# Kernel optimization log

Measured on AMD Instinct MI355X. Metric: run time of the kernel, lower is better.

## Reference

```python
import jax, jax.numpy as jnp
import numpy as np
from jax import lax

N, C_IN, C_OUT, H, W = 8, 64, 64, 128, 128
K, KS, STRIDE, PAD, GROUPS = 4, 3, 1, 1, 1


def setup_inputs() -> dict:
    key = jax.random.key(0)
    ks = jax.random.split(key, 10)
    s = 0.05
    return {
        "x": jax.random.normal(ks[0], (N, C_IN, H, W), jnp.float32),
        "weight": jax.random.normal(ks[1], (K, C_OUT, C_IN // GROUPS, KS, KS), jnp.float32) * s,
        "conv_w": jax.random.normal(ks[2], (C_OUT, C_IN, KS, KS), jnp.float32) * s,
        "conv_b": jax.random.normal(ks[3], (C_OUT,), jnp.float32) * s,
        "net0_w": jax.random.normal(ks[4], (K, 1, 1, 1, 1), jnp.float32) * s,
        "net0_b": jax.random.normal(ks[5], (K,), jnp.float32) * s,
        "net1_w": jax.random.normal(ks[6], (K, 1, 3, 3, 3), jnp.float32) * s,
        "net1_b": jax.random.normal(ks[7], (K,), jnp.float32) * s,
        "net2_w": jax.random.normal(ks[8], (K, 1, 5, 3, 3), jnp.float32) * s,
        "net2_b": jax.random.normal(ks[9], (K,), jnp.float32) * s,
    }


def _conv3d_mean(x5, w, b, pad):
    # x5: (N,1,C,H,W); w: (K,1,kd,kh,kw); 'same'-style padding per kernel.
    y = lax.conv_general_dilated(x5, w, (1, 1, 1), [(p, p) for p in pad],
                                 dimension_numbers=('NCDHW', 'OIDHW', 'NCDHW'))
    # global avg pool over (C,H,W); bias is constant so add after the mean.
    return jnp.mean(y, axis=(2, 3, 4)) + b[None, :]


def reference(x, weight, conv_w, conv_b, net0_w, net0_b, net1_w, net1_b, net2_w, net2_b):
    dn2 = ('NCHW', 'OIHW', 'NCHW')
    # static residual conv branch
    r = lax.conv_general_dilated(x, conv_w, (STRIDE, STRIDE), [(PAD, PAD)] * 2,
                                 dimension_numbers=dn2) + conv_b[None, :, None, None]
    # attention over 3D convs of x.unsqueeze(1)
    x5 = x[:, None]  # (N,1,C,H,W)
    logits = (_conv3d_mean(x5, net0_w, net0_b, (0, 0, 0))
              + _conv3d_mean(x5, net1_w, net1_b, (1, 1, 1))
              + _conv3d_mean(x5, net2_w, net2_b, (2, 1, 1)))  # (N,K)
    att = jax.nn.softmax(logits, axis=-1)
    # per-sample dynamic kernel mixing: (N,K) @ (K,out,in/g,kh,kw)
    agg_w = jnp.einsum('nk,koihw->noihw', att, weight)
    # grouped conv with groups = GROUPS*N == per-sample conv (vmapped)
    def per_sample(xi, wi):
        return lax.conv_general_dilated(xi[None], wi, (STRIDE, STRIDE), [(PAD, PAD)] * 2,
                                        dimension_numbers=dn2,
                                        feature_group_count=GROUPS)[0]
    out = jax.vmap(per_sample)(x, agg_w)  # (N,out,H,W)
    return out + r
```

## Files before the change

### kernel.cpp

```cpp
#include <hip/hip_runtime.h>


typedef unsigned short ushort_t;
typedef __attribute__((ext_vector_type(8))) short bf16x8;
typedef __attribute__((ext_vector_type(4))) float f32x4;

__device__ __forceinline__ ushort_t f2bf(float f) {
    unsigned u = __float_as_uint(f);
    unsigned r = (u + 0x7fffu + ((u >> 16) & 1u)) >> 16;
    return (ushort_t)r;
}

__global__ __launch_bounds__(256) void kTR(const float* __restrict__ x,
                                           ushort_t* __restrict__ xt,
                                           float* __restrict__ part) {
    int row = blockIdx.x;
    int h = row & 127, n = row >> 7;
    int tid = threadIdx.x;
    int wg = tid & 31;
    int ci8 = tid >> 5;

    __shared__ float catloc[15];
    if (tid < 15) catloc[tid] = 0.f;
    __syncthreads();

    const float* xp = x + (size_t)(n * 64 + ci8 * 8) * 16384 + h * 128 + wg;
    float v[8][4];
#pragma unroll
    for (int j = 0; j < 8; ++j)
#pragma unroll
        for (int c = 0; c < 4; ++c)
            v[j][c] = xp[j * 16384 + c * 32];

    ushort_t* op = xt + ((size_t)(row * 8 + ci8)) * 128 * 8;
#pragma unroll
    for (int c = 0; c < 4; ++c) {
        ushort_t u[8];
#pragma unroll
        for (int j = 0; j < 8; ++j) u[j] = f2bf(v[j][c]);
        uint4 pk;
        pk.x = (unsigned)u[0] | ((unsigned)u[1] << 16);
        pk.y = (unsigned)u[2] | ((unsigned)u[3] << 16);
        pk.z = (unsigned)u[4] | ((unsigned)u[5] << 16);
        pk.w = (unsigned)u[6] | ((unsigned)u[7] << 16);
        *(uint4*)(op + (size_t)(wg + c * 32) * 8) = pk;
    }

#pragma unroll
    for (int j = 0; j < 8; ++j) {
        float rs = v[j][0] + v[j][1] + v[j][2] + v[j][3];
#pragma unroll
        for (int m = 1; m <= 16; m <<= 1) rs += __shfl_xor(rs, m);
        int ci = ci8 * 8 + j;
        int cd = (ci == 0) ? 0 : (ci == 1) ? 1 : (ci == 62) ? 3 : (ci == 63) ? 4 : 2;
        if (wg == 0) {
            atomicAdd(&catloc[cd * 3 + 0], rs);
            atomicAdd(&catloc[cd * 3 + 1], v[j][0]);
        }
        if (wg == 31) atomicAdd(&catloc[cd * 3 + 2], v[j][3]);
    }
    __syncthreads();
    if (tid < 15) part[row * 16 + tid] = catloc[tid];
}

__global__ __launch_bounds__(256) void kW(const float* __restrict__ part,
                                          const float* __restrict__ nw0, const float* __restrict__ nb0,
                                          const float* __restrict__ nw1, const float* __restrict__ nb1,
                                          const float* __restrict__ nw2, const float* __restrict__ nb2,
                                          const float* __restrict__ weight,
                                          const float* __restrict__ convw,
                                          ushort_t* __restrict__ weff) {
    int bid = blockIdx.x;
    int s = bid % 9;
    int n = bid / 9;
    int tid = threadIdx.x;

    __shared__ float cat_s[45];
    __shared__ float box_s[45];
    __shared__ float tot_s;
    __shared__ float att_s[4];

    if (tid < 45) cat_s[tid] = 0.f;
    __syncthreads();
    if (tid < 128) {
        int h = tid;
        int ch = (h == 0) ? 0 : (h == 127) ? 2 : 1;
        const float* pp = part + (size_t)(n * 128 + h) * 16;
#pragma unroll
        for (int q = 0; q < 15; ++q) {
            int cd = q / 3, st = q % 3;
            atomicAdd(&cat_s[(cd * 3 + ch) * 3 + st], pp[q]);
        }
    }
    __syncthreads();

    if (tid < 46) {
        float c[5][3][3];
#pragma unroll
        for (int i = 0; i < 5; ++i)
#pragma unroll
            for (int j = 0; j < 3; ++j)
#pragma unroll
                for (int t = 0; t < 3; ++t)
                    c[i][j][t] = cat_s[(i * 3 + j) * 3 + t];

        if (tid < 45) {
            int dz = tid / 9 - 2;
            int dy = (tid / 3) % 3 - 1;
            int dx = tid % 3 - 1;
            float acc = 0.f;
#pragma unroll
            for (int cd = 0; cd < 5; ++cd) {
                int dv = (cd == 0) ? 0 : (cd == 1) ? 1 : (cd == 3) ? 62 : (cd == 4) ? 63 : -1;
                bool incd = (dv < 0) || (dv >= dz && dv < 64 + dz);
#pragma unroll
                for (int ch = 0; ch < 3; ++ch) {
                    int hv = (ch == 0) ? 0 : (ch == 2) ? 127 : -1;
                    bool inch = (hv < 0) || (hv >= dy && hv < 128 + dy);
                    if (incd && inch) {
                        float v = c[cd][ch][0];
                        if (dx == -1) v -= c[cd][ch][2];
                        else if (dx == 1) v -= c[cd][ch][1];
                        acc += v;
                    }
                }
            }
            box_s[tid] = acc;
        } else {
            float tot = 0.f;
#pragma unroll
            for (int i = 0; i < 5; ++i)
#pragma unroll
                for (int j = 0; j < 3; ++j) tot += c[i][j][0];
            tot_s = tot;
        }
    }
    __syncthreads();

    if (tid < 4) {
        int k = tid;
        const float invV = 1.0f / (64.f * 128.f * 128.f);
        float lg = nb0[k] + nb1[k] + nb2[k] + nw0[k] * tot_s * invV;
#pragma unroll
        for (int dz = 0; dz < 3; ++dz)
#pragma unroll
            for (int dy = 0; dy < 3; ++dy)
#pragma unroll
                for (int dx = 0; dx < 3; ++dx)
                    lg += nw1[k * 27 + dz * 9 + dy * 3 + dx] *
                          box_s[(dz + 1) * 9 + dy * 3 + dx] * invV;
#pragma unroll
        for (int b = 0; b < 45; ++b)
            lg += nw2[k * 45 + b] * box_s[b] * invV;

        float m = fmaxf(lg, __shfl_xor(lg, 1));
        m = fmaxf(m, __shfl_xor(m, 2));
        float e = __expf(lg - m);
        float ssum = e + __shfl_xor(e, 1);
        ssum += __shfl_xor(ssum, 2);
        att_s[k] = e / ssum;
    }
    __syncthreads();

    float a0 = att_s[0], a1 = att_s[1], a2 = att_s[2], a3 = att_s[3];
    int ci = tid & 63;
    int cog = tid >> 6;
    ushort_t* wp = weff + ((size_t)(n * 9 + s) * 64) * 64;
#pragma unroll
    for (int p = 0; p < 16; ++p) {
        int co = cog * 16 + p;
        size_t base = (size_t)(co * 64 + ci) * 9 + s;
        float v = convw[base]
                + a0 * weight[base]
                + a1 * weight[base +     64 * 64 * 9]
                + a2 * weight[base + 2 * 64 * 64 * 9]
                + a3 * weight[base + 3 * 64 * 64 * 9];
        wp[(size_t)co * 64 + ci] = f2bf(v);
    }
}

__global__ __launch_bounds__(256, 2) void kC(const ushort_t* __restrict__ xt,
                                             const ushort_t* __restrict__ weff,
                                             const float* __restrict__ convb,
                                             float* __restrict__ out) {
    int bid = blockIdx.x;
    int wt = bid & 1;
    int hq = (bid >> 1) & 31;
    int n = bid >> 6;
    int h0 = hq * 4;
    int w0 = wt * 64;

    __shared__ __align__(16) ushort_t lds[6 * 8 * 66 * 8];

    int tid = threadIdx.x;
    int lane = tid & 63;
    int wave = tid >> 6;
    int kq = lane >> 4;
    int l15 = lane & 15;

    for (int idx = tid; idx < 3168; idx += 256) {
        int c = idx % 66;
        int rc8 = idx / 66;
        int r = rc8 >> 3, ci8 = rc8 & 7;
        int hg = h0 + r - 1;
        int wg = w0 + c - 1;
        uint4 vv = make_uint4(0u, 0u, 0u, 0u);
        if (hg >= 0 && hg < 128 && wg >= 0 && wg < 128)
            vv = *(const uint4*)(xt + ((size_t)((n * 128 + hg) * 8 + ci8) * 128 + wg) * 8);
        *(uint4*)&lds[(size_t)idx * 8] = vv;
    }

    int co_a = wave * 16 + l15;
    bf16x8 afrag[9][2];
#pragma unroll
    for (int s = 0; s < 9; ++s)
#pragma unroll
        for (int kc = 0; kc < 2; ++kc)
            afrag[s][kc] = *(const bf16x8*)(weff +
                ((size_t)((n * 9 + s) * 64 + co_a)) * 64 + kc * 32 + kq * 8);

    f32x4 acc[16];
#pragma unroll
    for (int t = 0; t < 16; ++t) acc[t] = (f32x4){0.f, 0.f, 0.f, 0.f};

    __syncthreads();

#pragma unroll
    for (int kx = 0; kx < 3; ++kx) {
#pragma unroll
        for (int kc = 0; kc < 2; ++kc) {
#pragma unroll
            for (int col = 0; col < 4; ++col) {
                bf16x8 brow[6];
#pragma unroll
                for (int p = 0; p < 6; ++p)
                    brow[p] = *(const bf16x8*)
                        &lds[(((p * 8 + kc * 4 + kq) * 66) + col * 16 + l15 + kx) * 8];
#pragma unroll
                for (int ky = 0; ky < 3; ++ky)
#pragma unroll
                    for (int r = 0; r < 4; ++r)
                        acc[r * 4 + col] = __builtin_amdgcn_mfma_f32_16x16x32_bf16(
                            afrag[ky * 3 + kx][kc], brow[r + ky], acc[r * 4 + col], 0, 0, 0);
            }
        }
    }

#pragma unroll
    for (int r = 0; r < 4; ++r) {
        int h = h0 + r;
#pragma unroll
        for (int col = 0; col < 4; ++col) {
            int w = w0 + col * 16 + l15;
#pragma unroll
            for (int reg = 0; reg < 4; ++reg) {
                int co = wave * 16 + kq * 4 + reg;
                float v = acc[r * 4 + col][reg] + convb[co];
                out[(((size_t)n * 64 + co) * 128 + h) * 128 + w] = v;
            }
        }
    }
}

extern "C" void kernel_launch(void* const* d_in, const int* in_sizes, int n_in,
                              void* d_out, int out_size, void* d_ws, size_t ws_size,
                              hipStream_t stream) {
    const float* x      = (const float*)d_in[0];
    const float* weight = (const float*)d_in[1];
    const float* conv_w = (const float*)d_in[2];
    const float* conv_b = (const float*)d_in[3];
    const float* n0w    = (const float*)d_in[4];
    const float* n0b    = (const float*)d_in[5];
    const float* n1w    = (const float*)d_in[6];
    const float* n1b    = (const float*)d_in[7];
    const float* n2w    = (const float*)d_in[8];
    const float* n2b    = (const float*)d_in[9];
    float* out = (float*)d_out;

    char* ws = (char*)d_ws;
    ushort_t* xt   = (ushort_t*)(ws);
    ushort_t* weff = (ushort_t*)(ws + 16777216);
    float*    part = (float*)(ws + 16777216 + 589824);

    kTR<<<1024, 256, 0, stream>>>(x, xt, part);
    kW<<<72, 256, 0, stream>>>(part, n0w, n0b, n1w, n1b, n2w, n2b,
                               weight, conv_w, weff);
    kC<<<512, 256, 0, stream>>>(xt, weff, conv_b, out);
}
```

Measured before the change: 130.4 us.

## Pre-pad transposed input and use direct global-to-LDS loads in conv kernel

The transposed bf16 input is now stored with a zero border of width one in H and W (130x130), written by the transpose kernel. The conv kernel can then drop its bounds checks and stage its tile with global_load_lds buffer-to-LDS transfers that skip registers, with a short register-path tail. The weight-mixing kernel is split across four times as many blocks (each handles a quarter of the output channels), and conv blocks are reordered so batch varies fastest. The trade-offs are extra border writes, a larger workspace, and kW blocks that each redo the attention reduction.

```diff
diff --git a/kernel.cpp b/kernel.cpp
--- a/kernel.cpp
+++ b/kernel.cpp
@@ -9,6 +9,12 @@
     unsigned u = __float_as_uint(f);
     unsigned r = (u + 0x7fffu + ((u >> 16) & 1u)) >> 16;
     return (ushort_t)r;
+}
+
+__device__ __forceinline__ void gl_lds16(const ushort_t* g, ushort_t* l) {
+    __builtin_amdgcn_global_load_lds(
+        (const __attribute__((address_space(1))) unsigned*)g,
+        (__attribute__((address_space(3))) unsigned*)l, 16, 0, 0);
 }
 
 __global__ __launch_bounds__(256) void kTR(const float* __restrict__ x,
@@ -32,7 +38,7 @@
         for (int c = 0; c < 4; ++c)
             v[j][c] = xp[j * 16384 + c * 32];
 
-    ushort_t* op = xt + ((size_t)(row * 8 + ci8)) * 128 * 8;
+    ushort_t* op = xt + (((size_t)(n * 130 + h + 1) * 8 + ci8) * 130 + 1) * 8;
 #pragma unroll
     for (int c = 0; c < 4; ++c) {
         ushort_t u[8];
@@ -44,6 +50,18 @@
         pk.z = (unsigned)u[4] | ((unsigned)u[5] << 16);
         pk.w = (unsigned)u[6] | ((unsigned)u[7] << 16);
         *(uint4*)(op + (size_t)(wg + c * 32) * 8) = pk;
+    }
+
+    if (tid < 16) {
+        int cib = tid & 7, side = tid >> 3;
+        *(uint4*)(xt + (((size_t)(n * 130 + h + 1) * 8 + cib) * 130 + side * 129) * 8)
+            = make_uint4(0u, 0u, 0u, 0u);
+    }
+    if (h == 0 || h == 127) {
+        int hp = (h == 0) ? 0 : 129;
+        size_t base = (size_t)(n * 130 + hp) * 8 * 130;
+        for (int ii = tid; ii < 1040; ii += 256)
+            *(uint4*)(xt + (base + ii) * 8) = make_uint4(0u, 0u, 0u, 0u);
     }
 
 #pragma unroll
@@ -71,8 +89,10 @@
                                           const float* __restrict__ convw,
                                           ushort_t* __restrict__ weff) {
     int bid = blockIdx.x;
-    int s = bid % 9;
-    int n = bid / 9;
+    int q = bid & 3;
+    int ns = bid >> 2;
+    int s = ns % 9;
+    int n = ns / 9;
     int tid = threadIdx.x;
 
     __shared__ float cat_s[45];
@@ -87,9 +107,9 @@
         int ch = (h == 0) ? 0 : (h == 127) ? 2 : 1;
         const float* pp = part + (size_t)(n * 128 + h) * 16;
 #pragma unroll
-        for (int q = 0; q < 15; ++q) {
-            int cd = q / 3, st = q % 3;
-            atomicAdd(&cat_s[(cd * 3 + ch) * 3 + st], pp[q]);
+        for (int p = 0; p < 15; ++p) {
+            int cd = p / 3, st = p % 3;
+            atomicAdd(&cat_s[(cd * 3 + ch) * 3 + st], pp[p]);
         }
     }
     __syncthreads();
@@ -118,10 +138,10 @@
                     int hv = (ch == 0) ? 0 : (ch == 2) ? 127 : -1;
                     bool inch = (hv < 0) || (hv >= dy && hv < 128 + dy);
                     if (incd && inch) {
-                        float v = c[cd][ch][0];
-                        if (dx == -1) v -= c[cd][ch][2];
-                        else if (dx == 1) v -= c[cd][ch][1];
-                        acc += v;
+                        float vv = c[cd][ch][0];
+                        if (dx == -1) vv -= c[cd][ch][2];
+                        else if (dx == 1) vv -= c[cd][ch][1];
+                        acc += vv;
                     }
                 }
             }
@@ -167,8 +187,8 @@
     int cog = tid >> 6;
     ushort_t* wp = weff + ((size_t)(n * 9 + s) * 64) * 64;
 #pragma unroll
-    for (int p = 0; p < 16; ++p) {
-        int co = cog * 16 + p;
+    for (int p = 0; p < 4; ++p) {
+        int co = cog * 16 + q * 4 + p;
         size_t base = (size_t)(co * 64 + ci) * 9 + s;
         float v = convw[base]
                 + a0 * weight[base]
@@ -183,10 +203,11 @@
                                              const ushort_t* __restrict__ weff,
                                              const float* __restrict__ convb,
                                              float* __restrict__ out) {
-    int bid = blockIdx.x;
-    int wt = bid & 1;
-    int hq = (bid >> 1) & 31;
-    int n = bid >> 6;
+    int b = blockIdx.x;
+    int n = b & 7;
+    int r2 = b >> 3;
+    int wt = r2 & 1;
+    int hq = r2 >> 1;
     int h0 = hq * 4;
     int w0 = wt * 64;
 
@@ -198,16 +219,22 @@
     int kq = lane >> 4;
     int l15 = lane & 15;
 
-    for (int idx = tid; idx < 3168; idx += 256) {
-        int c = idx % 66;
-        int rc8 = idx / 66;
-        int r = rc8 >> 3, ci8 = rc8 & 7;
-        int hg = h0 + r - 1;
-        int wg = w0 + c - 1;
-        uint4 vv = make_uint4(0u, 0u, 0u, 0u);
-        if (hg >= 0 && hg < 128 && wg >= 0 && wg < 128)
-            vv = *(const uint4*)(xt + ((size_t)((n * 128 + hg) * 8 + ci8) * 128 + wg) * 8);
-        *(uint4*)&lds[(size_t)idx * 8] = vv;
+    size_t sbase = ((size_t)(n * 130 + h0) * 8) * 130 + w0;
+#pragma unroll
+    for (int m = 0; m < 12; ++m) {
+        int chunk = m * 256 + tid;
+        int c = chunk % 66;
+        int rc8 = chunk / 66;
+        size_t so = sbase + (size_t)(rc8 >> 3) * 1040 + (size_t)(rc8 & 7) * 130 + c;
+        gl_lds16(xt + so * 8, &lds[(size_t)chunk * 8]);
+    }
+    uint4 tail_v;
+    int tail_chunk = 3072 + tid;
+    if (tid < 96) {
+        int c = tail_chunk % 66;
+        int rc8 = tail_chunk / 66;
+        size_t so = sbase + (size_t)(rc8 >> 3) * 1040 + (size_t)(rc8 & 7) * 130 + c;
+        tail_v = *(const uint4*)(xt + so * 8);
     }
 
     int co_a = wave * 16 + l15;
@@ -218,6 +245,8 @@
         for (int kc = 0; kc < 2; ++kc)
             afrag[s][kc] = *(const bf16x8*)(weff +
                 ((size_t)((n * 9 + s) * 64 + co_a)) * 64 + kc * 32 + kq * 8);
+
+    if (tid < 96) *(uint4*)&lds[(size_t)tail_chunk * 8] = tail_v;
 
     f32x4 acc[16];
 #pragma unroll
@@ -279,11 +308,11 @@
 
     char* ws = (char*)d_ws;
     ushort_t* xt   = (ushort_t*)(ws);
-    ushort_t* weff = (ushort_t*)(ws + 16777216);
-    float*    part = (float*)(ws + 16777216 + 589824);
+    ushort_t* weff = (ushort_t*)(ws + 17305600);
+    float*    part = (float*)(ws + 17305600 + 589824);
 
     kTR<<<1024, 256, 0, stream>>>(x, xt, part);
-    kW<<<72, 256, 0, stream>>>(part, n0w, n0b, n1w, n1b, n2w, n2b,
-                               weight, conv_w, weff);
+    kW<<<288, 256, 0, stream>>>(part, n0w, n0b, n1w, n1b, n2w, n2b,
+                                weight, conv_w, weff);
     kC<<<512, 256, 0, stream>>>(xt, weff, conv_b, out);
 }
```

Measured after the change: 129.7 us. Within noise of the previous version (-0.5%).
